# Performance work log

Hardware: AMD Instinct MI355X
Metric: run time of the kernel (lower is better)

## Reference

```python
import jax, jax.numpy as jnp
import numpy as np

# dims: batch, nodes(sensors), window, embed, topk, MLP inter width
B, NODE, WIN, EMB, TOPK, INTER = 256, 512, 64, 64, 16, 512
NEG = 0.2      # LeakyReLU negative slope in GAT attention
EPS = 1e-5     # BatchNorm eps
N = B * NODE   # total graph nodes
E = N * TOPK   # total edges


def _bn(x, gamma, beta, axes):
    # training-mode BatchNorm: batch statistics (biased var), affine gamma/beta
    m = jnp.mean(x, axis=axes, keepdims=True)
    v = jnp.var(x, axis=axes, keepdims=True)
    return (x - m) * jax.lax.rsqrt(v + EPS) * gamma + beta


def setup_inputs() -> dict:
    key = jax.random.key(0)
    ks = jax.random.split(key, 12)
    sd = lambda k, shp, s: jax.random.normal(k, shp, jnp.float32) * s
    return {
        "data": jax.random.normal(ks[0], (B, NODE, WIN), jnp.float32),
        "org_edge_index": jax.random.randint(ks[1], (2, NODE), 0, NODE, dtype=jnp.int32),  # unused by forward
        "W_emb": sd(ks[2], (NODE, EMB), 0.1),          # nn.Embedding weight
        "W_lin": sd(ks[3], (EMB, WIN), 0.1),           # GraphLayer.lin (no bias)
        "att_i": sd(ks[4], (EMB,), 0.1),
        "att_j": sd(ks[5], (EMB,), 0.1),
        "att_em_i": sd(ks[6], (EMB,), 0.1),
        "att_em_j": sd(ks[7], (EMB,), 0.1),
        "b_gnn": jnp.zeros((EMB,), jnp.float32),       # GraphLayer bias
        "g_bn1": jnp.ones((EMB,), jnp.float32), "b_bn1": jnp.zeros((EMB,), jnp.float32),
        "g_bn2": jnp.ones((EMB,), jnp.float32), "b_bn2": jnp.zeros((EMB,), jnp.float32),
        "W1": sd(ks[8], (INTER, EMB), 0.05), "b1": jnp.zeros((INTER,), jnp.float32),
        "g_bn3": jnp.ones((INTER,), jnp.float32), "b_bn3": jnp.zeros((INTER,), jnp.float32),
        "W2": sd(ks[9], (1, INTER), 0.05), "b2": jnp.zeros((1,), jnp.float32),
    }


def reference(data, org_edge_index, W_emb, W_lin, att_i, att_j, att_em_i, att_em_j,
              b_gnn, g_bn1, b_bn1, g_bn2, b_bn2, W1, b1, g_bn3, b_bn3, W2, b2):
    x = data.reshape(N, WIN)

    # ---- graph structure learning: cosine-sim top-k on DETACHED embeddings ----
    w = jax.lax.stop_gradient(W_emb)
    nw = w * jax.lax.rsqrt(jnp.sum(w * w, axis=-1, keepdims=True))
    cos = nw @ nw.T                                  # [NODE, NODE]
    _, topk_idx = jax.lax.top_k(cos, TOPK)           # [NODE, TOPK]; diag==1 -> self in top-k,
                                                     # so remove+add self-loops is a no-op on the edge set
    offs = (jnp.arange(N // NODE) * NODE)[:, None]   # batch offsets
    src = (topk_idx.reshape(-1)[None, :] + offs).reshape(-1)                 # [E] source j
    dst = (jnp.repeat(jnp.arange(NODE), TOPK)[None, :] + offs).reshape(-1)   # [E] target i (sorted)

    # ---- GAT-style message passing (heads=1, concat=False) ----
    xl = x @ W_lin.T                                 # [N, EMB]
    # per-node attention scores for key = [Wx || embedding]
    s_i = xl @ att_i + jnp.tile(W_emb @ att_em_i, B)  # [N]
    s_j = xl @ att_j + jnp.tile(W_emb @ att_em_j, B)  # [N]
    alpha = s_i[dst] + s_j[src]                      # [E]
    alpha = jnp.where(alpha > 0, alpha, NEG * alpha)  # leaky_relu
    # segment softmax over edges grouped by target node
    amax = jax.ops.segment_max(alpha, dst, num_segments=N, indices_are_sorted=True)
    ex = jnp.exp(alpha - amax[dst])
    den = jax.ops.segment_sum(ex, dst, num_segments=N, indices_are_sorted=True)
    attw = ex / den[dst]                             # [E]
    agg = jax.ops.segment_sum(attw[:, None] * xl[src], dst,
                              num_segments=N, indices_are_sorted=True)  # [N, EMB]
    h = jax.nn.relu(_bn(agg + b_gnn, g_bn1, b_bn1, axes=0))             # GNNLayer bn+relu

    # ---- readout: mul by embedding, BN over channels, MLP head (dropout=eval/identity) ----
    z = h.reshape(B, NODE, EMB) * W_emb[None]        # [B, NODE, EMB]
    z = jax.nn.relu(_bn(z, g_bn2, b_bn2, axes=(0, 1)))
    z = jax.nn.relu(_bn(z @ W1.T + b1, g_bn3, b_bn3, axes=(0, 1)))      # [B, NODE, INTER]
    out = (z @ W2.T + b2).reshape(B, NODE)
    return out
```

## Files before the change

kernel.cpp:

```cpp
#include <hip/hip_runtime.h>
#include <hip/hip_bf16.h>

constexpr int BATCH = 256, NNODE = 512, WINW = 64, EMBD = 64, KTOP = 16, CIN = 512;
constexpr int NTOT = BATCH * NNODE;
constexpr float NEGS = 0.2f;
constexpr float EPSBN = 1e-5f;

typedef __attribute__((ext_vector_type(8))) short bf16x8;
typedef __attribute__((ext_vector_type(4))) float f32x4;

__device__ inline float bf2f(unsigned u16) {
  union { unsigned u; float f; } v; v.u = u16 << 16; return v.f;
}
__device__ inline unsigned short f2bf(float x) {
  union { float f; unsigned u; } v; v.f = x;
  unsigned r = v.u + 0x7fff + ((v.u >> 16) & 1);
  return (unsigned short)(r >> 16);
}

__global__ void k_prep(const float* __restrict__ W_emb,
                       const float* __restrict__ att_em_i,
                       const float* __restrict__ att_em_j,
                       float* __restrict__ nw, float* __restrict__ emb_si,
                       float* __restrict__ emb_sj) {
  int i = blockIdx.x, e = threadIdx.x;
  float w  = W_emb[i * EMBD + e];
  float sq = w * w;
  float si = w * att_em_i[e];
  float sj = w * att_em_j[e];
  for (int o = 32; o > 0; o >>= 1) {
    sq += __shfl_xor(sq, o);
    si += __shfl_xor(si, o);
    sj += __shfl_xor(sj, o);
  }
  nw[i * EMBD + e] = w * rsqrtf(sq);
  if (e == 0) { emb_si[i] = si; emb_sj[i] = sj; }
}

__global__ __launch_bounds__(256) void k_topk(const float* __restrict__ nw,
                                              int* __restrict__ topk) {
  __shared__ float nwi[EMBD];
  __shared__ float wbv[4];
  __shared__ int   wbi[4];
  __shared__ int   winner;
  int i = blockIdx.x, t = threadIdx.x, wv = t >> 6, ln = t & 63;
  if (t < EMBD) nwi[t] = nw[i * EMBD + t];
  __syncthreads();
  float v0 = 0.f, v1 = 0.f;
  #pragma unroll
  for (int k = 0; k < EMBD; k++) {
    v0 += nw[t * EMBD + k] * nwi[k];
    v1 += nw[(t + 256) * EMBD + k] * nwi[k];
  }
  for (int sel = 0; sel < KTOP; sel++) {
    float bv; int bi;
    if (v1 > v0) { bv = v1; bi = t + 256; } else { bv = v0; bi = t; }
    #pragma unroll
    for (int o = 1; o < 64; o <<= 1) {
      float ov = __shfl_xor(bv, o);
      int   oi = __shfl_xor(bi, o);
      if (ov > bv || (ov == bv && oi < bi)) { bv = ov; bi = oi; }
    }
    if (ln == 0) { wbv[wv] = bv; wbi[wv] = bi; }
    __syncthreads();
    if (t == 0) {
      float B = wbv[0]; int I = wbi[0];
      #pragma unroll
      for (int w = 1; w < 4; w++)
        if (wbv[w] > B || (wbv[w] == B && wbi[w] < I)) { B = wbv[w]; I = wbi[w]; }
      topk[i * KTOP + sel] = I;
      winner = I;
    }
    __syncthreads();
    int wi = winner;
    if (wi == t) v0 = -3.f;
    else if (wi == t + 256) v1 = -3.f;
  }
}

__global__ __launch_bounds__(1024) void k_fuse(
    const float* __restrict__ data, const float* __restrict__ W_lin,
    const float* __restrict__ att_i, const float* __restrict__ att_j,
    const float* __restrict__ emb_si, const float* __restrict__ emb_sj,
    const int* __restrict__ topk,
    float* __restrict__ agg, float* __restrict__ gsum1, float* __restrict__ gss1) {
  __shared__ float xl[NNODE * EMBD];
  __shared__ float ssi[NNODE];
  __shared__ float ssj[NNODE];
  __shared__ float redb[16 * 128];
  const int b = blockIdx.x;
  const int t = threadIdx.x, w = t >> 6, ln = t & 63;
  const int lm = ln & 15, lq = ln >> 4, kb = lq * 8;

  bf16x8 bfrag[4][2];
  float ai4[4], aj4[4];
  #pragma unroll
  for (int ti = 0; ti < 4; ti++) {
    int ch = ti * 16 + lm;
    ai4[ti] = att_i[ch]; aj4[ti] = att_j[ch];
    #pragma unroll
    for (int s = 0; s < 2; s++) {
      const float* wp = W_lin + ch * WINW + s * 32 + kb;
      float4 w0 = *(const float4*)wp;
      float4 w1 = *(const float4*)(wp + 4);
      bf16x8 f;
      f[0] = (short)f2bf(w0.x); f[1] = (short)f2bf(w0.y);
      f[2] = (short)f2bf(w0.z); f[3] = (short)f2bf(w0.w);
      f[4] = (short)f2bf(w1.x); f[5] = (short)f2bf(w1.y);
      f[6] = (short)f2bf(w1.z); f[7] = (short)f2bf(w1.w);
      bfrag[ti][s] = f;
    }
  }
  #pragma unroll
  for (int tt = 0; tt < 2; tt++) {
    int tile = w * 2 + tt;
    const float* dr = data + ((size_t)b * NNODE + tile * 16 + lm) * WINW + kb;
    f32x4 acc[4];
    #pragma unroll
    for (int ti = 0; ti < 4; ti++) acc[ti] = (f32x4){0.f, 0.f, 0.f, 0.f};
    #pragma unroll
    for (int s = 0; s < 2; s++) {
      float4 d0 = *(const float4*)(dr + s * 32);
      float4 d1 = *(const float4*)(dr + s * 32 + 4);
      bf16x8 af;
      af[0] = (short)f2bf(d0.x); af[1] = (short)f2bf(d0.y);
      af[2] = (short)f2bf(d0.z); af[3] = (short)f2bf(d0.w);
      af[4] = (short)f2bf(d1.x); af[5] = (short)f2bf(d1.y);
      af[6] = (short)f2bf(d1.z); af[7] = (short)f2bf(d1.w);
      #pragma unroll
      for (int ti = 0; ti < 4; ti++)
        acc[ti] = __builtin_amdgcn_mfma_f32_16x16x32_bf16(af, bfrag[ti][s], acc[ti], 0, 0, 0);
    }
    #pragma unroll
    for (int r = 0; r < 4; r++) {
      int nd = tile * 16 + lq * 4 + r;
      float si = 0.f, sj = 0.f;
      #pragma unroll
      for (int ti = 0; ti < 4; ti++) {
        float v = acc[ti][r];
        xl[nd * EMBD + ti * 16 + lm] = v;
        si += v * ai4[ti];
        sj += v * aj4[ti];
      }
      si += __shfl_xor(si, 1); si += __shfl_xor(si, 2);
      si += __shfl_xor(si, 4); si += __shfl_xor(si, 8);
      sj += __shfl_xor(sj, 1); sj += __shfl_xor(sj, 2);
      sj += __shfl_xor(sj, 4); sj += __shfl_xor(sj, 8);
      if (lm == 0) { ssi[nd] = si + emb_si[nd]; ssj[nd] = sj + emb_sj[nd]; }
    }
  }
  __syncthreads();
  const int nd4 = ln >> 4, l4 = ln & 15;
  float psx = 0.f, psy = 0.f, psz = 0.f, psw = 0.f;
  float qsx = 0.f, qsy = 0.f, qsz = 0.f, qsw = 0.f;
  for (int it = 0; it < 8; it++) {
    int node = w * 32 + it * 4 + nd4;
    const int4* tp = (const int4*)(topk + node * KTOP);
    int4 i0 = tp[0], i1 = tp[1], i2 = tp[2], i3 = tp[3];
    int idx[16] = {i0.x, i0.y, i0.z, i0.w, i1.x, i1.y, i1.z, i1.w,
                   i2.x, i2.y, i2.z, i2.w, i3.x, i3.y, i3.z, i3.w};
    float sid = ssi[node];
    float al[16], mx = -1e30f;
    #pragma unroll
    for (int k = 0; k < KTOP; k++) {
      float a = sid + ssj[idx[k]];
      a = a > 0.f ? a : NEGS * a;
      al[k] = a;
      mx = fmaxf(mx, a);
    }
    float den = 0.f;
    #pragma unroll
    for (int k = 0; k < KTOP; k++) { al[k] = __expf(al[k] - mx); den += al[k]; }
    float inv = 1.f / den;
    float ax = 0.f, ay = 0.f, az = 0.f, aw = 0.f;
    #pragma unroll
    for (int k = 0; k < KTOP; k++) {
      float4 v = *(const float4*)&xl[idx[k] * EMBD + l4 * 4];
      ax += al[k] * v.x; ay += al[k] * v.y; az += al[k] * v.z; aw += al[k] * v.w;
    }
    ax *= inv; ay *= inv; az *= inv; aw *= inv;
    float4 st = {ax, ay, az, aw};
    *(float4*)(agg + ((size_t)b * NNODE + node) * EMBD + l4 * 4) = st;
    psx += ax; psy += ay; psz += az; psw += aw;
    qsx += ax * ax; qsy += ay * ay; qsz += az * az; qsw += aw * aw;
  }
  #pragma unroll
  for (int o = 16; o <= 32; o <<= 1) {
    psx += __shfl_xor(psx, o); psy += __shfl_xor(psy, o);
    psz += __shfl_xor(psz, o); psw += __shfl_xor(psw, o);
    qsx += __shfl_xor(qsx, o); qsy += __shfl_xor(qsy, o);
    qsz += __shfl_xor(qsz, o); qsw += __shfl_xor(qsw, o);
  }
  if (ln < 16) {
    float4 a = {psx, psy, psz, psw};
    float4 q = {qsx, qsy, qsz, qsw};
    *(float4*)&redb[w * 128 + ln * 4] = a;
    *(float4*)&redb[w * 128 + 64 + ln * 4] = q;
  }
  __syncthreads();
  if (t < 64) {
    float s = 0.f;
    #pragma unroll
    for (int w16 = 0; w16 < 16; w16++) s += redb[w16 * 128 + t];
    atomicAdd(&gsum1[t], s);
  } else if (t < 128) {
    int e = t - 64;
    float s = 0.f;
    #pragma unroll
    for (int w16 = 0; w16 < 16; w16++) s += redb[w16 * 128 + 64 + e];
    atomicAdd(&gss1[e], s);
  }
}

__global__ void k_fin(const float* __restrict__ gsum, const float* __restrict__ gss,
                      const float* __restrict__ g, const float* __restrict__ bb,
                      float* __restrict__ a, float* __restrict__ c, int C) {
  int e = blockIdx.x * blockDim.x + threadIdx.x;
  if (e >= C) return;
  const float invn = 1.f / (float)NTOT;
  float m = gsum[e] * invn;
  float v = gss[e] * invn - m * m;
  float aa = g[e] * rsqrtf(v + EPSBN);
  a[e] = aa;
  c[e] = bb[e] - m * aa;
}

__global__ __launch_bounds__(256) void k_zstats2(
    const float* __restrict__ agg, const float* __restrict__ W_emb,
    const float* __restrict__ a1, const float* __restrict__ c1,
    unsigned* __restrict__ zp, float* __restrict__ gsum2,
    float* __restrict__ gss2) {
  __shared__ float red[4][8][32];
  int t = threadIdx.x;
  int gid = blockIdx.x * 256 + t;
  int p = t & 31;
  int c0 = 2 * p;
  float a10 = a1[c0], a11 = a1[c0 + 1], c10 = c1[c0], c11 = c1[c0 + 1];
  const float2* agg2 = (const float2*)agg;
  const float2* we2  = (const float2*)W_emb;
  float ps0 = 0.f, ps1 = 0.f, q0 = 0.f, q1 = 0.f;
  int stride = gridDim.x * 256;
  for (int idx = gid; idx < NTOT * 32; idx += stride) {
    float2 v = agg2[idx];
    int node = (idx >> 5) & (NNODE - 1);
    float2 w = we2[node * 32 + p];
    float z0 = v.x * a10 + c10; z0 = z0 > 0.f ? z0 : 0.f; z0 *= w.x;
    float z1 = v.y * a11 + c11; z1 = z1 > 0.f ? z1 : 0.f; z1 *= w.y;
    zp[idx] = (unsigned)f2bf(z0) | ((unsigned)f2bf(z1) << 16);
    ps0 += z0; q0 += z0 * z0; ps1 += z1; q1 += z1 * z1;
  }
  int g = t >> 5;
  red[0][g][p] = ps0; red[1][g][p] = ps1; red[2][g][p] = q0; red[3][g][p] = q1;
  __syncthreads();
  if (t < 128) {
    int v = t >> 5, p2 = t & 31;
    float s = 0.f;
    #pragma unroll
    for (int k = 0; k < 8; k++) s += red[v][k][p2];
    float* dst = (v & 2) ? gss2 : gsum2;
    atomicAdd(&dst[2 * p2 + (v & 1)], s);
  }
}

__global__ __launch_bounds__(256) void k_gram(
    const unsigned* __restrict__ zp, const float* __restrict__ a2,
    const float* __restrict__ c2, float* __restrict__ Gpart,
    float* __restrict__ hpart) {
  __shared__ float hst[128 * 68];
  __shared__ float red[4][64];
  const int t = threadIdx.x, wv = t >> 6, ln = t & 63;
  const int i0 = 8 * (ln & 7), j0 = 8 * (ln >> 3);
  const int p = t & 31, c0 = 2 * p;
  float a20 = a2[c0], a21 = a2[c0 + 1], c20 = c2[c0], c21 = c2[c0 + 1];
  float ga[8][8];
  #pragma unroll
  for (int a = 0; a < 8; a++)
    #pragma unroll
    for (int b = 0; b < 8; b++) ga[a][b] = 0.f;
  float hs[8] = {0.f, 0.f, 0.f, 0.f, 0.f, 0.f, 0.f, 0.f};
  const int rowbase = blockIdx.x * 256;
  for (int st = 0; st < 2; st++) {
    int base32 = (rowbase + st * 128) * 32;
    unsigned us[16];
    #pragma unroll
    for (int s = 0; s < 16; s++) us[s] = zp[base32 + s * 256 + t];
    __syncthreads();
    #pragma unroll
    for (int s = 0; s < 16; s++) {
      int row = s * 8 + (t >> 5);
      float z0 = bf2f(us[s] & 0xffffu);
      float z1 = bf2f(us[s] >> 16);
      float h0 = z0 * a20 + c20; h0 = h0 > 0.f ? h0 : 0.f;
      float h1 = z1 * a21 + c21; h1 = h1 > 0.f ? h1 : 0.f;
      *(float2*)&hst[row * 68 + c0] = make_float2(h0, h1);
    }
    __syncthreads();
    for (int q = 0; q < 32; q++) {
      int r = wv * 32 + q;
      float4 hi0 = *(const float4*)&hst[r * 68 + i0];
      float4 hi1 = *(const float4*)&hst[r * 68 + i0 + 4];
      float4 hj0 = *(const float4*)&hst[r * 68 + j0];
      float4 hj1 = *(const float4*)&hst[r * 68 + j0 + 4];
      float hia[8] = {hi0.x, hi0.y, hi0.z, hi0.w, hi1.x, hi1.y, hi1.z, hi1.w};
      float hja[8] = {hj0.x, hj0.y, hj0.z, hj0.w, hj1.x, hj1.y, hj1.z, hj1.w};
      #pragma unroll
      for (int a = 0; a < 8; a++) {
        float hv = hia[a];
        hs[a] += hv;
        #pragma unroll
        for (int b = 0; b < 8; b++) ga[a][b] += hv * hja[b];
      }
    }
  }
  __syncthreads();
  float* G_lds = hst;
  for (int k = t; k < 4096; k += 256) G_lds[k] = 0.f;
  __syncthreads();
  for (int w = 0; w < 4; w++) {
    if (wv == w) {
      #pragma unroll
      for (int a = 0; a < 8; a++)
        #pragma unroll
        for (int bb = 0; bb < 8; bb++) {
          int b = (bb + (ln & 7)) & 7;
          G_lds[(i0 + a) * 64 + j0 + b] += ga[a][b];
        }
    }
    __syncthreads();
  }
  for (int k = t; k < 4096; k += 256) Gpart[(size_t)blockIdx.x * 4096 + k] = G_lds[k];
  #pragma unroll
  for (int k = 0; k < 8; k++) {
    float v = hs[k];
    v += __shfl_xor(v, 8); v += __shfl_xor(v, 16); v += __shfl_xor(v, 32);
    hs[k] = v * 0.125f;
  }
  if (ln < 8) {
    #pragma unroll
    for (int k = 0; k < 8; k++) red[wv][ln * 8 + k] = hs[k];
  }
  __syncthreads();
  if (t < 64)
    hpart[(size_t)blockIdx.x * 64 + t] = red[0][t] + red[1][t] + red[2][t] + red[3][t];
}

__global__ __launch_bounds__(256) void k_gred(const float* __restrict__ Gpart,
                                              const float* __restrict__ hpart,
                                              float* __restrict__ G,
                                              float* __restrict__ hsum) {
  int wi = blockIdx.x * 256 + threadIdx.x;
  if (wi < 32768) {
    int e = wi & 4095, seg = wi >> 12;
    float s = 0.f;
    #pragma unroll 8
    for (int k = 0; k < 64; k++) s += Gpart[(size_t)((seg << 6) + k) * 4096 + e];
    atomicAdd(&G[e], s);
  } else {
    int wi2 = wi - 32768;
    int e = wi2 & 63, seg = wi2 >> 6;
    float s = 0.f;
    #pragma unroll 8
    for (int k = 0; k < 64; k++) s += hpart[(size_t)((seg << 6) + k) * 64 + e];
    atomicAdd(&hsum[e], s);
  }
}

__global__ __launch_bounds__(64) void k_fin3q(
    const float* __restrict__ G, const float* __restrict__ hsum,
    const float* __restrict__ W1, const float* __restrict__ b1,
    const float* __restrict__ g3, const float* __restrict__ b3,
    float* __restrict__ a3, float* __restrict__ c3) {
  __shared__ float sw[64];
  int c = blockIdx.x, i = threadIdx.x;
  float w1i = W1[c * 64 + i];
  sw[i] = w1i;
  __syncthreads();
  float gw = 0.f;
  #pragma unroll
  for (int j = 0; j < 64; j++) gw += G[j * 64 + i] * sw[j];
  float t1 = w1i * gw;
  float t2 = w1i * hsum[i];
  for (int o = 32; o > 0; o >>= 1) { t1 += __shfl_xor(t1, o); t2 += __shfl_xor(t2, o); }
  if (i == 0) {
    float b1c = b1[c];
    const float fn = (float)NTOT, invn = 1.f / fn;
    float sum3 = t2 + fn * b1c;
    float ss3  = t1 + 2.f * b1c * t2 + fn * b1c * b1c;
    float m = sum3 * invn;
    float v = ss3 * invn - m * m;
    float aa = g3[c] * rsqrtf(v + EPSBN);
    a3[c] = aa;
    c3[c] = b3[c] - m * aa;
  }
}

__global__ __launch_bounds__(512) void k_gout2(
    const unsigned* __restrict__ zpu, const float* __restrict__ W1,
    const float* __restrict__ b1, const float* __restrict__ a2,
    const float* __restrict__ c2, const float* __restrict__ a3,
    const float* __restrict__ c3, const float* __restrict__ W2,
    const float* __restrict__ b2, float* __restrict__ out) {
  __shared__ uint4 hstage[64 * 8];
  __shared__ float opart[64][9];
  const int t = threadIdx.x, wv = t >> 6, ln = t & 63;
  const int lm = ln & 15, lq = ln >> 4, kb = lq * 8;
  const int srow = t >> 3, sg = t & 7;
  const uint4* zp4 = (const uint4*)zpu;

  float a2v[8], c2v[8];
  #pragma unroll
  for (int j = 0; j < 8; j++) { a2v[j] = a2[sg * 8 + j]; c2v[j] = c2[sg * 8 + j]; }

  bf16x8 bfrag[4][2];
  float b1c[4], a3c[4], c3c[4], w2c[4];
  #pragma unroll
  for (int nt = 0; nt < 4; nt++) {
    int col = wv * 64 + nt * 16 + lm;
    b1c[nt] = b1[col]; a3c[nt] = a3[col]; c3c[nt] = c3[col]; w2c[nt] = W2[col];
    #pragma unroll
    for (int s = 0; s < 2; s++) {
      const float* wp = W1 + col * EMBD + s * 32 + kb;
      float4 w0 = *(const float4*)wp;
      float4 w1 = *(const float4*)(wp + 4);
      bf16x8 f;
      f[0] = (short)f2bf(w0.x); f[1] = (short)f2bf(w0.y);
      f[2] = (short)f2bf(w0.z); f[3] = (short)f2bf(w0.w);
      f[4] = (short)f2bf(w1.x); f[5] = (short)f2bf(w1.y);
      f[6] = (short)f2bf(w1.z); f[7] = (short)f2bf(w1.w);
      bfrag[nt][s] = f;
    }
  }
  float b2v = b2[0];
  const int rowbase = blockIdx.x * 512;
  for (int st = 0; st < 8; st++) {
    int base = rowbase + st * 64;
    uint4 u = zp4[(size_t)(base + srow) * 8 + sg];
    float v[8] = {bf2f(u.x & 0xffffu), bf2f(u.x >> 16),
                  bf2f(u.y & 0xffffu), bf2f(u.y >> 16),
                  bf2f(u.z & 0xffffu), bf2f(u.z >> 16),
                  bf2f(u.w & 0xffffu), bf2f(u.w >> 16)};
    unsigned hp[4];
    #pragma unroll
    for (int j = 0; j < 4; j++) {
      float h0 = v[2 * j] * a2v[2 * j] + c2v[2 * j];     h0 = h0 > 0.f ? h0 : 0.f;
      float h1 = v[2 * j + 1] * a2v[2 * j + 1] + c2v[2 * j + 1]; h1 = h1 > 0.f ? h1 : 0.f;
      hp[j] = (unsigned)f2bf(h0) | ((unsigned)f2bf(h1) << 16);
    }
    __syncthreads();
    hstage[srow * 8 + (sg ^ (srow & 7))] = make_uint4(hp[0], hp[1], hp[2], hp[3]);
    __syncthreads();
    f32x4 acc[4][4];
    #pragma unroll
    for (int mt = 0; mt < 4; mt++)
      #pragma unroll
      for (int nt = 0; nt < 4; nt++) acc[mt][nt] = (f32x4){0.f, 0.f, 0.f, 0.f};
    const bf16x8* hb = (const bf16x8*)hstage;
    #pragma unroll
    for (int s = 0; s < 2; s++) {
      bf16x8 af[4];
      #pragma unroll
      for (int mt = 0; mt < 4; mt++) {
        int row = mt * 16 + lm;
        af[mt] = hb[row * 8 + ((s * 4 + lq) ^ (row & 7))];
      }
      #pragma unroll
      for (int mt = 0; mt < 4; mt++)
        #pragma unroll
        for (int nt = 0; nt < 4; nt++)
          acc[mt][nt] = __builtin_amdgcn_mfma_f32_16x16x32_bf16(af[mt], bfrag[nt][s], acc[mt][nt], 0, 0, 0);
    }
    #pragma unroll
    for (int mt = 0; mt < 4; mt++) {
      #pragma unroll
      for (int r = 0; r < 4; r++) {
        float p = 0.f;
        #pragma unroll
        for (int nt = 0; nt < 4; nt++) {
          float z2 = acc[mt][nt][r] + b1c[nt];
          float y = z2 * a3c[nt] + c3c[nt];
          y = y > 0.f ? y : 0.f;
          p += y * w2c[nt];
        }
        p += __shfl_xor(p, 1); p += __shfl_xor(p, 2);
        p += __shfl_xor(p, 4); p += __shfl_xor(p, 8);
        if (lm == 0) opart[mt * 16 + lq * 4 + r][wv] = p;
      }
    }
    __syncthreads();
    if (t < 64) {
      float s = 0.f;
      #pragma unroll
      for (int w = 0; w < 8; w++) s += opart[t][w];
      out[base + t] = s + b2v;
    }
  }
}

extern "C" void kernel_launch(void* const* d_in, const int* in_sizes, int n_in,
                              void* d_out, int out_size, void* d_ws, size_t ws_size,
                              hipStream_t stream) {
  const float* data     = (const float*)d_in[0];
  const float* W_emb    = (const float*)d_in[2];
  const float* W_lin    = (const float*)d_in[3];
  const float* att_i    = (const float*)d_in[4];
  const float* att_j    = (const float*)d_in[5];
  const float* att_em_i = (const float*)d_in[6];
  const float* att_em_j = (const float*)d_in[7];
  const float* g_bn1    = (const float*)d_in[9];
  const float* b_bn1    = (const float*)d_in[10];
  const float* g_bn2    = (const float*)d_in[11];
  const float* b_bn2    = (const float*)d_in[12];
  const float* W1       = (const float*)d_in[13];
  const float* b1       = (const float*)d_in[14];
  const float* g_bn3    = (const float*)d_in[15];
  const float* b_bn3    = (const float*)d_in[16];
  const float* W2       = (const float*)d_in[17];
  const float* b2       = (const float*)d_in[18];
  float* out = (float*)d_out;

  char* p = (char*)d_ws;
  auto alloc = [&](size_t bytes) {
    void* r = (void*)p;
    p += (bytes + 255) & ~(size_t)255;
    return r;
  };
  float*    agg   = (float*)alloc((size_t)NTOT * EMBD * 4);
  unsigned* zb    = (unsigned*)alloc((size_t)NTOT * EMBD * 2);
  float*    Gpart = (float*)alloc((size_t)512 * 4096 * 4);
  float*    hpart = (float*)alloc((size_t)512 * 64 * 4);
  float*    nw    = (float*)alloc((size_t)NNODE * EMBD * 4);
  float*    emb_si = (float*)alloc(NNODE * 4);
  float*    emb_sj = (float*)alloc(NNODE * 4);
  int*      topk   = (int*)alloc(NNODE * KTOP * 4);
  float*    stats  = (float*)alloc(4416 * 4);
  float*    coefs  = (float*)alloc(1280 * 4);

  float* gsum1 = stats;       float* gss1 = stats + 64;
  float* gsum2 = stats + 128; float* gss2 = stats + 192;
  float* G     = stats + 256; float* hsum = stats + 4352;
  float* a1 = coefs;       float* c1 = coefs + 64;
  float* a2 = coefs + 128; float* c2 = coefs + 192;
  float* a3 = coefs + 256; float* c3 = coefs + 768;

  hipMemsetAsync(stats, 0, 4416 * 4, stream);

  k_prep<<<NNODE, 64, 0, stream>>>(W_emb, att_em_i, att_em_j, nw, emb_si, emb_sj);
  k_topk<<<NNODE, 256, 0, stream>>>(nw, topk);
  k_fuse<<<BATCH, 1024, 0, stream>>>(data, W_lin, att_i, att_j, emb_si, emb_sj,
                                     topk, agg, gsum1, gss1);
  k_fin<<<1, 64, 0, stream>>>(gsum1, gss1, g_bn1, b_bn1, a1, c1, EMBD);
  k_zstats2<<<1024, 256, 0, stream>>>(agg, W_emb, a1, c1, zb, gsum2, gss2);
  k_fin<<<1, 64, 0, stream>>>(gsum2, gss2, g_bn2, b_bn2, a2, c2, EMBD);
  k_gram<<<512, 256, 0, stream>>>(zb, a2, c2, Gpart, hpart);
  k_gred<<<130, 256, 0, stream>>>(Gpart, hpart, G, hsum);
  k_fin3q<<<CIN, 64, 0, stream>>>(G, hsum, W1, b1, g_bn3, b_bn3, a3, c3);
  k_gout2<<<256, 512, 0, stream>>>(zb, W1, b1, a2, c2, a3, c3, W2, b2, out);
}
```

Before: 285.4 us.

## Store agg in bf16, precompute h in gram, restructure output GEMM with atomics

The aggregation output is now written as packed bf16 instead of fp32, which halves that intermediate's write and read traffic. k_gram additionally writes the BN2-normalized h tensor in bf16. A new output kernel reads those fragments straight from global memory into MFMA operands, with no LDS staging or recompute. Each wave now handles a slice of the INTER columns for a 16-row tile and atomically adds its partial dot product into a zeroed output. This costs an extra h write, a memset of the output, lower precision for agg, and many atomics.

```diff
diff --git a/kernel.cpp b/kernel.cpp
--- a/kernel.cpp
+++ b/kernel.cpp
@@ -8,6 +8,8 @@
 
 typedef __attribute__((ext_vector_type(8))) short bf16x8;
 typedef __attribute__((ext_vector_type(4))) float f32x4;
+
+union U8 { uint4 u; bf16x8 b; };
 
 __device__ inline float bf2f(unsigned u16) {
   union { unsigned u; float f; } v; v.u = u16 << 16; return v.f;
@@ -83,7 +85,8 @@
     const float* __restrict__ att_i, const float* __restrict__ att_j,
     const float* __restrict__ emb_si, const float* __restrict__ emb_sj,
     const int* __restrict__ topk,
-    float* __restrict__ agg, float* __restrict__ gsum1, float* __restrict__ gss1) {
+    unsigned* __restrict__ aggb, float* __restrict__ gsum1,
+    float* __restrict__ gss1) {
   __shared__ float xl[NNODE * EMBD];
   __shared__ float ssi[NNODE];
   __shared__ float ssj[NNODE];
@@ -179,8 +182,9 @@
       ax += al[k] * v.x; ay += al[k] * v.y; az += al[k] * v.z; aw += al[k] * v.w;
     }
     ax *= inv; ay *= inv; az *= inv; aw *= inv;
-    float4 st = {ax, ay, az, aw};
-    *(float4*)(agg + ((size_t)b * NNODE + node) * EMBD + l4 * 4) = st;
+    unsigned u0 = (unsigned)f2bf(ax) | ((unsigned)f2bf(ay) << 16);
+    unsigned u1 = (unsigned)f2bf(az) | ((unsigned)f2bf(aw) << 16);
+    *(uint2*)(aggb + (((size_t)b * NNODE + node) << 5) + l4 * 2) = make_uint2(u0, u1);
     psx += ax; psy += ay; psz += az; psw += aw;
     qsx += ax * ax; qsy += ay * ay; qsz += az * az; qsw += aw * aw;
   }
@@ -226,7 +230,7 @@
 }
 
 __global__ __launch_bounds__(256) void k_zstats2(
-    const float* __restrict__ agg, const float* __restrict__ W_emb,
+    const unsigned* __restrict__ aggb, const float* __restrict__ W_emb,
     const float* __restrict__ a1, const float* __restrict__ c1,
     unsigned* __restrict__ zp, float* __restrict__ gsum2,
     float* __restrict__ gss2) {
@@ -236,16 +240,16 @@
   int p = t & 31;
   int c0 = 2 * p;
   float a10 = a1[c0], a11 = a1[c0 + 1], c10 = c1[c0], c11 = c1[c0 + 1];
-  const float2* agg2 = (const float2*)agg;
   const float2* we2  = (const float2*)W_emb;
   float ps0 = 0.f, ps1 = 0.f, q0 = 0.f, q1 = 0.f;
   int stride = gridDim.x * 256;
   for (int idx = gid; idx < NTOT * 32; idx += stride) {
-    float2 v = agg2[idx];
+    unsigned u = aggb[idx];
+    float vx = bf2f(u & 0xffffu), vy = bf2f(u >> 16);
     int node = (idx >> 5) & (NNODE - 1);
     float2 w = we2[node * 32 + p];
-    float z0 = v.x * a10 + c10; z0 = z0 > 0.f ? z0 : 0.f; z0 *= w.x;
-    float z1 = v.y * a11 + c11; z1 = z1 > 0.f ? z1 : 0.f; z1 *= w.y;
+    float z0 = vx * a10 + c10; z0 = z0 > 0.f ? z0 : 0.f; z0 *= w.x;
+    float z1 = vy * a11 + c11; z1 = z1 > 0.f ? z1 : 0.f; z1 *= w.y;
     zp[idx] = (unsigned)f2bf(z0) | ((unsigned)f2bf(z1) << 16);
     ps0 += z0; q0 += z0 * z0; ps1 += z1; q1 += z1 * z1;
   }
@@ -265,7 +269,7 @@
 __global__ __launch_bounds__(256) void k_gram(
     const unsigned* __restrict__ zp, const float* __restrict__ a2,
     const float* __restrict__ c2, float* __restrict__ Gpart,
-    float* __restrict__ hpart) {
+    float* __restrict__ hpart, unsigned* __restrict__ hb) {
   __shared__ float hst[128 * 68];
   __shared__ float red[4][64];
   const int t = threadIdx.x, wv = t >> 6, ln = t & 63;
@@ -293,6 +297,8 @@
       float h0 = z0 * a20 + c20; h0 = h0 > 0.f ? h0 : 0.f;
       float h1 = z1 * a21 + c21; h1 = h1 > 0.f ? h1 : 0.f;
       *(float2*)&hst[row * 68 + c0] = make_float2(h0, h1);
+      hb[(size_t)(rowbase + st * 128 + row) * 32 + p] =
+          (unsigned)f2bf(h0) | ((unsigned)f2bf(h1) << 16);
     }
     __syncthreads();
     for (int q = 0; q < 32; q++) {
@@ -394,23 +400,13 @@
   }
 }
 
-__global__ __launch_bounds__(512) void k_gout2(
-    const unsigned* __restrict__ zpu, const float* __restrict__ W1,
-    const float* __restrict__ b1, const float* __restrict__ a2,
-    const float* __restrict__ c2, const float* __restrict__ a3,
+__global__ __launch_bounds__(512) void k_gout3(
+    const unsigned* __restrict__ hb, const float* __restrict__ W1,
+    const float* __restrict__ b1, const float* __restrict__ a3,
     const float* __restrict__ c3, const float* __restrict__ W2,
     const float* __restrict__ b2, float* __restrict__ out) {
-  __shared__ uint4 hstage[64 * 8];
-  __shared__ float opart[64][9];
   const int t = threadIdx.x, wv = t >> 6, ln = t & 63;
   const int lm = ln & 15, lq = ln >> 4, kb = lq * 8;
-  const int srow = t >> 3, sg = t & 7;
-  const uint4* zp4 = (const uint4*)zpu;
-
-  float a2v[8], c2v[8];
-  #pragma unroll
-  for (int j = 0; j < 8; j++) { a2v[j] = a2[sg * 8 + j]; c2v[j] = c2[sg * 8 + j]; }
-
   bf16x8 bfrag[4][2];
   float b1c[4], a3c[4], c3c[4], w2c[4];
   #pragma unroll
@@ -431,67 +427,37 @@
     }
   }
   float b2v = b2[0];
-  const int rowbase = blockIdx.x * 512;
-  for (int st = 0; st < 8; st++) {
-    int base = rowbase + st * 64;
-    uint4 u = zp4[(size_t)(base + srow) * 8 + sg];
-    float v[8] = {bf2f(u.x & 0xffffu), bf2f(u.x >> 16),
-                  bf2f(u.y & 0xffffu), bf2f(u.y >> 16),
-                  bf2f(u.z & 0xffffu), bf2f(u.z >> 16),
-                  bf2f(u.w & 0xffffu), bf2f(u.w >> 16)};
-    unsigned hp[4];
-    #pragma unroll
-    for (int j = 0; j < 4; j++) {
-      float h0 = v[2 * j] * a2v[2 * j] + c2v[2 * j];     h0 = h0 > 0.f ? h0 : 0.f;
-      float h1 = v[2 * j + 1] * a2v[2 * j + 1] + c2v[2 * j + 1]; h1 = h1 > 0.f ? h1 : 0.f;
-      hp[j] = (unsigned)f2bf(h0) | ((unsigned)f2bf(h1) << 16);
-    }
-    __syncthreads();
-    hstage[srow * 8 + (sg ^ (srow & 7))] = make_uint4(hp[0], hp[1], hp[2], hp[3]);
-    __syncthreads();
-    f32x4 acc[4][4];
-    #pragma unroll
-    for (int mt = 0; mt < 4; mt++)
+  const uint4* h4 = (const uint4*)hb;
+  for (int tile = blockIdx.x; tile < NTOT / 16; tile += gridDim.x) {
+    int rowbase = tile * 16;
+    U8 ua, ub;
+    ua.u = h4[(size_t)(rowbase + lm) * 8 + lq];
+    ub.u = h4[(size_t)(rowbase + lm) * 8 + 4 + lq];
+    f32x4 acc[4];
+    #pragma unroll
+    for (int nt = 0; nt < 4; nt++) acc[nt] = (f32x4){0.f, 0.f, 0.f, 0.f};
+    #pragma unroll
+    for (int nt = 0; nt < 4; nt++)
+      acc[nt] = __builtin_amdgcn_mfma_f32_16x16x32_bf16(ua.b, bfrag[nt][0], acc[nt], 0, 0, 0);
+    #pragma unroll
+    for (int nt = 0; nt < 4; nt++)
+      acc[nt] = __builtin_amdgcn_mfma_f32_16x16x32_bf16(ub.b, bfrag[nt][1], acc[nt], 0, 0, 0);
+    #pragma unroll
+    for (int r = 0; r < 4; r++) {
+      float p = 0.f;
       #pragma unroll
-      for (int nt = 0; nt < 4; nt++) acc[mt][nt] = (f32x4){0.f, 0.f, 0.f, 0.f};
-    const bf16x8* hb = (const bf16x8*)hstage;
-    #pragma unroll
-    for (int s = 0; s < 2; s++) {
-      bf16x8 af[4];
-      #pragma unroll
-      for (int mt = 0; mt < 4; mt++) {
-        int row = mt * 16 + lm;
-        af[mt] = hb[row * 8 + ((s * 4 + lq) ^ (row & 7))];
+      for (int nt = 0; nt < 4; nt++) {
+        float z2 = acc[nt][r] + b1c[nt];
+        float y = z2 * a3c[nt] + c3c[nt];
+        y = y > 0.f ? y : 0.f;
+        p += y * w2c[nt];
       }
-      #pragma unroll
-      for (int mt = 0; mt < 4; mt++)
-        #pragma unroll
-        for (int nt = 0; nt < 4; nt++)
-          acc[mt][nt] = __builtin_amdgcn_mfma_f32_16x16x32_bf16(af[mt], bfrag[nt][s], acc[mt][nt], 0, 0, 0);
-    }
-    #pragma unroll
-    for (int mt = 0; mt < 4; mt++) {
-      #pragma unroll
-      for (int r = 0; r < 4; r++) {
-        float p = 0.f;
-        #pragma unroll
-        for (int nt = 0; nt < 4; nt++) {
-          float z2 = acc[mt][nt][r] + b1c[nt];
-          float y = z2 * a3c[nt] + c3c[nt];
-          y = y > 0.f ? y : 0.f;
-          p += y * w2c[nt];
-        }
-        p += __shfl_xor(p, 1); p += __shfl_xor(p, 2);
-        p += __shfl_xor(p, 4); p += __shfl_xor(p, 8);
-        if (lm == 0) opart[mt * 16 + lq * 4 + r][wv] = p;
+      p += __shfl_xor(p, 1); p += __shfl_xor(p, 2);
+      p += __shfl_xor(p, 4); p += __shfl_xor(p, 8);
+      if (lm == 0) {
+        if (wv == 0) p += b2v;
+        atomicAdd(&out[rowbase + lq * 4 + r], p);
       }
-    }
-    __syncthreads();
-    if (t < 64) {
-      float s = 0.f;
-      #pragma unroll
-      for (int w = 0; w < 8; w++) s += opart[t][w];
-      out[base + t] = s + b2v;
     }
   }
 }
@@ -524,8 +490,9 @@
     p += (bytes + 255) & ~(size_t)255;
     return r;
   };
-  float*    agg   = (float*)alloc((size_t)NTOT * EMBD * 4);
+  unsigned* aggb  = (unsigned*)alloc((size_t)NTOT * EMBD * 2);
   unsigned* zb    = (unsigned*)alloc((size_t)NTOT * EMBD * 2);
+  unsigned* hb    = (unsigned*)alloc((size_t)NTOT * EMBD * 2);
   float*    Gpart = (float*)alloc((size_t)512 * 4096 * 4);
   float*    hpart = (float*)alloc((size_t)512 * 64 * 4);
   float*    nw    = (float*)alloc((size_t)NNODE * EMBD * 4);
@@ -543,16 +510,17 @@
   float* a3 = coefs + 256; float* c3 = coefs + 768;
 
   hipMemsetAsync(stats, 0, 4416 * 4, stream);
+  hipMemsetAsync(out, 0, (size_t)NTOT * 4, stream);
 
   k_prep<<<NNODE, 64, 0, stream>>>(W_emb, att_em_i, att_em_j, nw, emb_si, emb_sj);
   k_topk<<<NNODE, 256, 0, stream>>>(nw, topk);
   k_fuse<<<BATCH, 1024, 0, stream>>>(data, W_lin, att_i, att_j, emb_si, emb_sj,
-                                     topk, agg, gsum1, gss1);
+                                     topk, aggb, gsum1, gss1);
   k_fin<<<1, 64, 0, stream>>>(gsum1, gss1, g_bn1, b_bn1, a1, c1, EMBD);
-  k_zstats2<<<1024, 256, 0, stream>>>(agg, W_emb, a1, c1, zb, gsum2, gss2);
+  k_zstats2<<<1024, 256, 0, stream>>>(aggb, W_emb, a1, c1, zb, gsum2, gss2);
   k_fin<<<1, 64, 0, stream>>>(gsum2, gss2, g_bn2, b_bn2, a2, c2, EMBD);
-  k_gram<<<512, 256, 0, stream>>>(zb, a2, c2, Gpart, hpart);
+  k_gram<<<512, 256, 0, stream>>>(zb, a2, c2, Gpart, hpart, hb);
   k_gred<<<130, 256, 0, stream>>>(Gpart, hpart, G, hsum);
   k_fin3q<<<CIN, 64, 0, stream>>>(G, hsum, W1, b1, g_bn3, b_bn3, a3, c3);
-  k_gout2<<<256, 512, 0, stream>>>(zb, W1, b1, a2, c2, a3, c3, W2, b2, out);
-}
+  k_gout3<<<512, 512, 0, stream>>>(hb, W1, b1, a3, c3, W2, b2, out);
+}
```

Measured after the change: 283.0 us. Within noise of the previous version (-0.8%).
